# Kernel tuning notes

Hardware: AMD Instinct MI355X
Metric: run time of the kernel (lower is better)

## Reference

```python
import jax, jax.numpy as jnp
import numpy as np

D_MODEL = 2048
N_HEADS = 16
D_HEAD = D_MODEL // N_HEADS
ROPE_BASE = 10000.0
B, L = 2, 2048


def _rope(x, positions):
    # x: [B, H, L, dh]; positions: [B, L] (float)
    dh = x.shape[-1]
    inv_freq = 1.0 / (ROPE_BASE ** (jnp.arange(0, dh, 2, dtype=jnp.float32) / dh))  # [dh/2]
    freqs = positions[:, :, None].astype(jnp.float32) * inv_freq  # [B, L, dh/2]
    cos = jnp.cos(freqs)[:, None, :, :]  # [B, 1, L, dh/2]
    sin = jnp.sin(freqs)[:, None, :, :]
    x1 = x[..., 0::2]
    x2 = x[..., 1::2]
    even = x1 * cos - x2 * sin
    odd = x1 * sin + x2 * cos
    # re-interleave: [..., dh/2, 2] -> [..., dh]
    return jnp.stack([even, odd], axis=-1).reshape(x.shape)


def setup_inputs() -> dict:
    key = jax.random.key(0)
    ks = jax.random.split(key, 5)
    std = 0.02
    x = jax.random.normal(ks[0], (B, L, D_MODEL), dtype=jnp.float32)
    Wq = jax.random.normal(ks[1], (D_MODEL, D_MODEL), dtype=jnp.float32) * std
    Wk = jax.random.normal(ks[2], (D_MODEL, D_MODEL), dtype=jnp.float32) * std
    Wv = jax.random.normal(ks[3], (D_MODEL, D_MODEL), dtype=jnp.float32) * std
    Wo = jax.random.normal(ks[4], (D_MODEL, D_MODEL), dtype=jnp.float32) * (std / np.sqrt(2.0))
    positions = jnp.broadcast_to(jnp.arange(L, dtype=jnp.int32)[None, :], (B, L))
    return {"x": x, "positions": positions, "Wq": Wq, "Wk": Wk, "Wv": Wv, "Wo": Wo}


def reference(x, positions, Wq, Wk, Wv, Wo):
    Bx, Lx, D = x.shape
    H, dh = N_HEADS, D_HEAD
    scale = 1.0 / np.sqrt(dh)
    # torch nn.Linear: y = x @ W.T (weights are [out, in])
    Q = (x @ Wq.T).reshape(Bx, Lx, H, dh).transpose(0, 2, 1, 3)  # [B,H,L,dh]
    K = (x @ Wk.T).reshape(Bx, Lx, H, dh).transpose(0, 2, 1, 3)
    V = (x @ Wv.T).reshape(Bx, Lx, H, dh).transpose(0, 2, 1, 3)
    Q = _rope(Q, positions)
    K = _rope(K, positions)
    scores = jnp.einsum('bhqd,bhkd->bhqk', Q, K) * scale  # [B,H,L,L]
    causal_mask = jnp.triu(jnp.full((Lx, Lx), -jnp.inf, dtype=scores.dtype), k=1)
    scores = scores + causal_mask[None, None, :, :]
    attn = jax.nn.softmax(scores, axis=-1)
    out = jnp.einsum('bhqk,bhkd->bhqd', attn, V)  # [B,H,L,dh]
    out = out.transpose(0, 2, 1, 3).reshape(Bx, Lx, D)
    return out @ Wo.T
```

## Files before the change

kernel.cpp:

```cpp
#include <hip/hip_runtime.h>
#include <hip/hip_bf16.h>

typedef __bf16 bf16;
typedef __bf16 bf16x8 __attribute__((ext_vector_type(8)));
typedef __bf16 bf16x4 __attribute__((ext_vector_type(4)));
typedef float f32x4 __attribute__((ext_vector_type(4)));

#define DM 2048
#define LL 2048
#define NB 2
#define NH 16
#define DH 128

__device__ __forceinline__ void gload_lds16(const void* g, void* l) {
  auto gp = (__attribute__((address_space(1))) void*)(const_cast<void*>(g));
  auto lp = (__attribute__((address_space(3))) void*)l;
  __builtin_amdgcn_global_load_lds(gp, lp, 16, 0, 0);
}

__global__ __launch_bounds__(256) void convert_kernel(
    const float* __restrict__ x, const float* __restrict__ wq,
    const float* __restrict__ wk, const float* __restrict__ wv,
    const float* __restrict__ wo,
    bf16* __restrict__ xb, bf16* __restrict__ wqb, bf16* __restrict__ wkb,
    bf16* __restrict__ wvb, bf16* __restrict__ wob) {
  int i4 = blockIdx.x * 256 + threadIdx.x;
  const float* src;
  bf16* dst;
  int off;
  if (i4 < 2097152) {
    src = x; dst = xb; off = i4;
  } else {
    int t = i4 - 2097152;
    int a = t >> 20;
    off = t & 1048575;
    src = (a == 0) ? wq : (a == 1) ? wk : (a == 2) ? wv : wo;
    dst = (a == 0) ? wqb : (a == 1) ? wkb : (a == 2) ? wvb : wob;
  }
  float4 v = ((const float4*)src)[off];
  bf16x4 o = {(bf16)v.x, (bf16)v.y, (bf16)v.z, (bf16)v.w};
  ((bf16x4*)dst)[off] = o;
}

__global__ __launch_bounds__(256) void rope_table_kernel(float2* __restrict__ cs) {
  int idx = blockIdx.x * 256 + threadIdx.x;
  int pos = idx >> 6, i = idx & 63;
  float inv = powf(10000.0f, -(float)(2 * i) / 128.0f);
  float f = (float)pos * inv;
  cs[idx] = make_float2(cosf(f), sinf(f));
}

template <int MODE>
__global__ __launch_bounds__(256) void gemm_kernel(
    const bf16* __restrict__ A, const bf16* __restrict__ B0,
    const bf16* __restrict__ B1, const bf16* __restrict__ B2,
    bf16* __restrict__ Qh, bf16* __restrict__ Kh, bf16* __restrict__ VT,
    float* __restrict__ Cout, const int* __restrict__ positions,
    const float2* __restrict__ cs) {
  __shared__ __align__(16) bf16 As[128 * 32];
  __shared__ __align__(16) bf16 Bs[128 * 32];
  const int tid = threadIdx.x;
  const int lane = tid & 63;
  const int w = tid >> 6;
  const int wr = w >> 1, wc = w & 1;
  const int lr = lane & 15, lg = lane >> 4;
  const int brow = blockIdx.x * 128;
  const int bcol = blockIdx.y * 128;
  const int z = (MODE == 0) ? (int)blockIdx.z : 0;
  const bf16* Bt = (MODE == 1) ? B0 : (z == 0 ? B0 : (z == 1 ? B1 : B2));

  f32x4 acc[4][4];
#pragma unroll
  for (int m = 0; m < 4; ++m)
#pragma unroll
    for (int n = 0; n < 4; ++n) acc[m][n] = (f32x4){0.f, 0.f, 0.f, 0.f};

  for (int kt = 0; kt < DM / 32; ++kt) {
    __syncthreads();
#pragma unroll
    for (int p = 0; p < 2; ++p) {
      int slot = p * 256 + tid;
      int row = slot >> 2, kq = slot & 3;
      gload_lds16(A + (size_t)(brow + row) * DM + kt * 32 + kq * 8,
                  As + (size_t)(p * 256 + w * 64) * 8);
      gload_lds16(Bt + (size_t)(bcol + row) * DM + kt * 32 + kq * 8,
                  Bs + (size_t)(p * 256 + w * 64) * 8);
    }
    __syncthreads();
    bf16x8 afr[4], bfr[4];
#pragma unroll
    for (int m = 0; m < 4; ++m)
      afr[m] = *(const bf16x8*)(As + (wr * 64 + m * 16 + lr) * 32 + lg * 8);
#pragma unroll
    for (int n = 0; n < 4; ++n)
      bfr[n] = *(const bf16x8*)(Bs + (wc * 64 + n * 16 + lr) * 32 + lg * 8);
#pragma unroll
    for (int m = 0; m < 4; ++m)
#pragma unroll
      for (int n = 0; n < 4; ++n)
        acc[m][n] = __builtin_amdgcn_mfma_f32_16x16x32_bf16(afr[m], bfr[n],
                                                            acc[m][n], 0, 0, 0);
  }

  if (MODE == 1) {
#pragma unroll
    for (int m = 0; m < 4; ++m)
#pragma unroll
      for (int r = 0; r < 4; ++r) {
        int gr = brow + wr * 64 + m * 16 + lg * 4 + r;
#pragma unroll
        for (int n = 0; n < 4; ++n) {
          int j = bcol + wc * 64 + n * 16 + lr;
          Cout[(size_t)gr * DM + j] = acc[m][n][r];
        }
      }
  } else if (z < 2) {
    bf16* Dst = (z == 0) ? Qh : Kh;
#pragma unroll
    for (int m = 0; m < 4; ++m)
#pragma unroll
      for (int r = 0; r < 4; ++r) {
        int gr = brow + wr * 64 + m * 16 + lg * 4 + r;
        int b = gr >> 11, l = gr & (LL - 1);
        int pos = positions[gr];
#pragma unroll
        for (int n = 0; n < 4; ++n) {
          int j = bcol + wc * 64 + n * 16 + lr;
          float v = acc[m][n][r];
          float part = __shfl_xor(v, 1);
          int d = j & 127;
          float2 csv = cs[pos * 64 + (d >> 1)];
          float res = (j & 1) ? (part * csv.y + v * csv.x)
                              : (v * csv.x - part * csv.y);
          Dst[((size_t)(b * NH + (j >> 7)) * LL + l) * DH + d] = (bf16)res;
        }
      }
  } else {
#pragma unroll
    for (int m = 0; m < 4; ++m) {
      int gr0 = brow + wr * 64 + m * 16 + lg * 4;
      int b = gr0 >> 11, l0 = gr0 & (LL - 1);
#pragma unroll
      for (int n = 0; n < 4; ++n) {
        int j = bcol + wc * 64 + n * 16 + lr;
        int d = j & 127, h = j >> 7;
        bf16x4 o = {(bf16)acc[m][n][0], (bf16)acc[m][n][1], (bf16)acc[m][n][2],
                    (bf16)acc[m][n][3]};
        *(bf16x4*)(VT + ((size_t)(b * NH + h) * DH + d) * LL + l0) = o;
      }
    }
  }
}

__global__ __launch_bounds__(256) void attn_kernel(const bf16* __restrict__ Qh,
                                                   const bf16* __restrict__ Kh,
                                                   const bf16* __restrict__ VT,
                                                   bf16* __restrict__ AO) {
  __shared__ __align__(16) bf16 Ks[64 * 128];
  __shared__ __align__(16) bf16 Vs[128 * 64];
  __shared__ __align__(16) bf16 Ps[4][16 * 64];
  const int tid = threadIdx.x;
  const int lane = tid & 63;
  const int w = tid >> 6;
  const int lr = lane & 15, lg = lane >> 4;
  const int bid = blockIdx.x;
  const int xcd = bid & 7;
  const int local = bid >> 3;
  const int bh = xcd * 4 + (local & 3);
  const int q0 = (local >> 2) * 64;
  const int qr0 = q0 + w * 16;
  const bf16* Qb = Qh + (size_t)bh * LL * DH;
  const bf16* Kb = Kh + (size_t)bh * LL * DH;
  const bf16* Vb = VT + (size_t)bh * DH * LL;

  bf16x8 qf[4];
#pragma unroll
  for (int dk = 0; dk < 4; ++dk)
    qf[dk] = *(const bf16x8*)(Qb + (size_t)(qr0 + lr) * DH + dk * 32 + lg * 8);

  float mx[4], ssum[4];
  f32x4 oacc[8];
#pragma unroll
  for (int r = 0; r < 4; ++r) {
    mx[r] = -1e30f;
    ssum[r] = 0.f;
  }
#pragma unroll
  for (int f = 0; f < 8; ++f) oacc[f] = (f32x4){0.f, 0.f, 0.f, 0.f};

  const float scale = 0.08838834764831845f;
  const int kvend = q0 + 64;
  for (int kv0 = 0; kv0 < kvend; kv0 += 64) {
    __syncthreads();
#pragma unroll
    for (int rr = 0; rr < 4; ++rr) {
      int slot = rr * 256 + tid;
      int row = slot >> 4, c = slot & 15;
      gload_lds16(Kb + (size_t)(kv0 + row) * DH + ((c ^ (row & 7)) * 8),
                  Ks + (size_t)(rr * 256 + w * 64) * 8);
    }
#pragma unroll
    for (int rr = 0; rr < 4; ++rr) {
      int slot = rr * 256 + tid;
      int row = slot >> 3, c = slot & 7;
      gload_lds16(Vb + (size_t)row * LL + kv0 + ((c ^ (row & 7)) * 8),
                  Vs + (size_t)(rr * 256 + w * 64) * 8);
    }
    __syncthreads();
    if (kv0 <= qr0 + 15) {
      f32x4 s[4];
#pragma unroll
      for (int n = 0; n < 4; ++n) s[n] = (f32x4){0.f, 0.f, 0.f, 0.f};
#pragma unroll
      for (int n = 0; n < 4; ++n)
#pragma unroll
        for (int dk = 0; dk < 4; ++dk) {
          bf16x8 kf = *(const bf16x8*)(Ks + (n * 16 + lr) * 128 +
                                       (((dk * 4 + lg) ^ (lr & 7)) * 8));
          s[n] = __builtin_amdgcn_mfma_f32_16x16x32_bf16(qf[dk], kf, s[n], 0, 0, 0);
        }
#pragma unroll
      for (int n = 0; n < 4; ++n)
#pragma unroll
        for (int r = 0; r < 4; ++r) {
          int c = kv0 + n * 16 + lr;
          int q = qr0 + lg * 4 + r;
          if (c > q) s[n][r] = -1e30f;
        }
      float pm[4];
      bool ok = true;
#pragma unroll
      for (int r = 0; r < 4; ++r) {
        float tm = fmaxf(fmaxf(s[0][r], s[1][r]), fmaxf(s[2][r], s[3][r]));
        tm = fmaxf(tm, __shfl_xor(tm, 1));
        tm = fmaxf(tm, __shfl_xor(tm, 2));
        tm = fmaxf(tm, __shfl_xor(tm, 4));
        tm = fmaxf(tm, __shfl_xor(tm, 8));
        pm[r] = tm;
        ok = ok && (tm <= mx[r] + 90.0f);
      }
      if (!__all(ok)) {
        float al[4];
#pragma unroll
        for (int r = 0; r < 4; ++r) {
          float mn = fmaxf(mx[r], pm[r]);
          al[r] = __expf((mx[r] - mn) * scale);
          mx[r] = mn;
          ssum[r] *= al[r];
        }
#pragma unroll
        for (int f = 0; f < 8; ++f)
#pragma unroll
          for (int r = 0; r < 4; ++r) oacc[f][r] *= al[r];
      }
#pragma unroll
      for (int r = 0; r < 4; ++r) {
        float t = 0.f;
#pragma unroll
        for (int n = 0; n < 4; ++n) {
          float e = __expf((s[n][r] - mx[r]) * scale);
          s[n][r] = e;
          t += e;
        }
        t += __shfl_xor(t, 1);
        t += __shfl_xor(t, 2);
        t += __shfl_xor(t, 4);
        t += __shfl_xor(t, 8);
        ssum[r] += t;
      }
      bf16* pw = &Ps[w][0];
#pragma unroll
      for (int n = 0; n < 4; ++n)
#pragma unroll
        for (int r = 0; r < 4; ++r) {
          int row = lg * 4 + r;
          int ch = (n * 2 + (lr >> 3)) ^ (row & 7);
          pw[row * 64 + ch * 8 + (lr & 7)] = (bf16)s[n][r];
        }
      asm volatile("s_waitcnt lgkmcnt(0)" ::: "memory");
      __builtin_amdgcn_sched_barrier(0);
#pragma unroll
      for (int kt = 0; kt < 2; ++kt) {
        bf16x8 pf = *(const bf16x8*)(pw + lr * 64 +
                                     (((kt * 4 + lg) ^ (lr & 7)) * 8));
#pragma unroll
        for (int f = 0; f < 8; ++f) {
          bf16x8 vf = *(const bf16x8*)(Vs + (f * 16 + lr) * 64 +
                                       (((kt * 4 + lg) ^ (lr & 7)) * 8));
          oacc[f] = __builtin_amdgcn_mfma_f32_16x16x32_bf16(pf, vf, oacc[f], 0, 0, 0);
        }
      }
    }
  }
  const int b = bh >> 4, h = bh & 15;
#pragma unroll
  for (int f = 0; f < 8; ++f)
#pragma unroll
    for (int r = 0; r < 4; ++r) {
      int q = qr0 + lg * 4 + r;
      float val = oacc[f][r] / ssum[r];
      AO[((size_t)(b * LL + q)) * DM + h * DH + f * 16 + lr] = (bf16)val;
    }
}

extern "C" void kernel_launch(void* const* d_in, const int* in_sizes, int n_in,
                              void* d_out, int out_size, void* d_ws,
                              size_t ws_size, hipStream_t stream) {
  const float* x = (const float*)d_in[0];
  const int* positions = (const int*)d_in[1];
  const float* Wq = (const float*)d_in[2];
  const float* Wk = (const float*)d_in[3];
  const float* Wv = (const float*)d_in[4];
  const float* Wo = (const float*)d_in[5];
  float* out = (float*)d_out;
  char* ws = (char*)d_ws;
  const size_t MB = (size_t)1 << 20;
  bf16* xb = (bf16*)(ws + 0 * MB);
  bf16* wqb = (bf16*)(ws + 16 * MB);
  bf16* wkb = (bf16*)(ws + 24 * MB);
  bf16* wvb = (bf16*)(ws + 32 * MB);
  bf16* wob = (bf16*)(ws + 40 * MB);
  bf16* Qh = (bf16*)(ws + 48 * MB);
  bf16* Kh = (bf16*)(ws + 64 * MB);
  bf16* VTb = (bf16*)(ws + 80 * MB);
  bf16* AO = (bf16*)(ws + 96 * MB);
  float2* cs = (float2*)(ws + 112 * MB);

  convert_kernel<<<dim3(24576), dim3(256), 0, stream>>>(
      x, Wq, Wk, Wv, Wo, xb, wqb, wkb, wvb, wob);
  rope_table_kernel<<<dim3(512), dim3(256), 0, stream>>>(cs);
  gemm_kernel<0><<<dim3(32, 16, 3), dim3(256), 0, stream>>>(
      xb, wqb, wkb, wvb, Qh, Kh, VTb, nullptr, positions, cs);
  attn_kernel<<<dim3(1024), dim3(256), 0, stream>>>(Qh, Kh, VTb, AO);
  gemm_kernel<1><<<dim3(32, 16, 1), dim3(256), 0, stream>>>(
      AO, wob, nullptr, nullptr, nullptr, nullptr, nullptr, out, nullptr,
      nullptr);
}
```

Measured before the change: 450.8 us.

## Double attention query tile per block to reuse K/V tiles across 128 queries

```diff
diff --git a/kernel.cpp b/kernel.cpp
--- a/kernel.cpp
+++ b/kernel.cpp
@@ -158,7 +158,7 @@
                                                    bf16* __restrict__ AO) {
   __shared__ __align__(16) bf16 Ks[64 * 128];
   __shared__ __align__(16) bf16 Vs[128 * 64];
-  __shared__ __align__(16) bf16 Ps[4][16 * 64];
+  __shared__ __align__(16) bf16 Ps[4][32 * 64];
   const int tid = threadIdx.x;
   const int lane = tid & 63;
   const int w = tid >> 6;
@@ -167,29 +167,35 @@
   const int xcd = bid & 7;
   const int local = bid >> 3;
   const int bh = xcd * 4 + (local & 3);
-  const int q0 = (local >> 2) * 64;
-  const int qr0 = q0 + w * 16;
+  const int q0 = (local >> 2) * 128;
+  const int qr0 = q0 + w * 32;
   const bf16* Qb = Qh + (size_t)bh * LL * DH;
   const bf16* Kb = Kh + (size_t)bh * LL * DH;
   const bf16* Vb = VT + (size_t)bh * DH * LL;
 
-  bf16x8 qf[4];
-#pragma unroll
-  for (int dk = 0; dk < 4; ++dk)
-    qf[dk] = *(const bf16x8*)(Qb + (size_t)(qr0 + lr) * DH + dk * 32 + lg * 8);
-
-  float mx[4], ssum[4];
-  f32x4 oacc[8];
-#pragma unroll
-  for (int r = 0; r < 4; ++r) {
-    mx[r] = -1e30f;
-    ssum[r] = 0.f;
-  }
-#pragma unroll
-  for (int f = 0; f < 8; ++f) oacc[f] = (f32x4){0.f, 0.f, 0.f, 0.f};
+  bf16x8 qf[2][4];
+#pragma unroll
+  for (int m = 0; m < 2; ++m)
+#pragma unroll
+    for (int dk = 0; dk < 4; ++dk)
+      qf[m][dk] = *(const bf16x8*)(Qb + (size_t)(qr0 + m * 16 + lr) * DH +
+                                   dk * 32 + lg * 8);
+
+  float mx[2][4], ssum[2][4];
+  f32x4 oacc[2][8];
+#pragma unroll
+  for (int m = 0; m < 2; ++m) {
+#pragma unroll
+    for (int r = 0; r < 4; ++r) {
+      mx[m][r] = -1e30f;
+      ssum[m][r] = 0.f;
+    }
+#pragma unroll
+    for (int f = 0; f < 8; ++f) oacc[m][f] = (f32x4){0.f, 0.f, 0.f, 0.f};
+  }
 
   const float scale = 0.08838834764831845f;
-  const int kvend = q0 + 64;
+  const int kvend = q0 + 128;
   for (int kv0 = 0; kv0 < kvend; kv0 += 64) {
     __syncthreads();
 #pragma unroll
@@ -207,100 +213,120 @@
                   Vs + (size_t)(rr * 256 + w * 64) * 8);
     }
     __syncthreads();
-    if (kv0 <= qr0 + 15) {
-      f32x4 s[4];
-#pragma unroll
-      for (int n = 0; n < 4; ++n) s[n] = (f32x4){0.f, 0.f, 0.f, 0.f};
+    if (kv0 <= qr0 + 31) {
+      f32x4 s[2][4];
+#pragma unroll
+      for (int m = 0; m < 2; ++m)
+#pragma unroll
+        for (int n = 0; n < 4; ++n) s[m][n] = (f32x4){0.f, 0.f, 0.f, 0.f};
 #pragma unroll
       for (int n = 0; n < 4; ++n)
 #pragma unroll
         for (int dk = 0; dk < 4; ++dk) {
           bf16x8 kf = *(const bf16x8*)(Ks + (n * 16 + lr) * 128 +
                                        (((dk * 4 + lg) ^ (lr & 7)) * 8));
-          s[n] = __builtin_amdgcn_mfma_f32_16x16x32_bf16(qf[dk], kf, s[n], 0, 0, 0);
-        }
-#pragma unroll
-      for (int n = 0; n < 4; ++n)
+          s[0][n] = __builtin_amdgcn_mfma_f32_16x16x32_bf16(qf[0][dk], kf,
+                                                            s[0][n], 0, 0, 0);
+          s[1][n] = __builtin_amdgcn_mfma_f32_16x16x32_bf16(qf[1][dk], kf,
+                                                            s[1][n], 0, 0, 0);
+        }
+#pragma unroll
+      for (int m = 0; m < 2; ++m)
+#pragma unroll
+        for (int n = 0; n < 4; ++n)
+#pragma unroll
+          for (int r = 0; r < 4; ++r) {
+            int c = kv0 + n * 16 + lr;
+            int q = qr0 + m * 16 + lg * 4 + r;
+            if (c > q) s[m][n][r] = -1e30f;
+          }
+      float pm[2][4];
+      bool ok = true;
+#pragma unroll
+      for (int m = 0; m < 2; ++m)
 #pragma unroll
         for (int r = 0; r < 4; ++r) {
-          int c = kv0 + n * 16 + lr;
-          int q = qr0 + lg * 4 + r;
-          if (c > q) s[n][r] = -1e30f;
-        }
-      float pm[4];
-      bool ok = true;
-#pragma unroll
-      for (int r = 0; r < 4; ++r) {
-        float tm = fmaxf(fmaxf(s[0][r], s[1][r]), fmaxf(s[2][r], s[3][r]));
-        tm = fmaxf(tm, __shfl_xor(tm, 1));
-        tm = fmaxf(tm, __shfl_xor(tm, 2));
-        tm = fmaxf(tm, __shfl_xor(tm, 4));
-        tm = fmaxf(tm, __shfl_xor(tm, 8));
-        pm[r] = tm;
-        ok = ok && (tm <= mx[r] + 90.0f);
-      }
+          float tm = fmaxf(fmaxf(s[m][0][r], s[m][1][r]),
+                           fmaxf(s[m][2][r], s[m][3][r]));
+          tm = fmaxf(tm, __shfl_xor(tm, 1));
+          tm = fmaxf(tm, __shfl_xor(tm, 2));
+          tm = fmaxf(tm, __shfl_xor(tm, 4));
+          tm = fmaxf(tm, __shfl_xor(tm, 8));
+          pm[m][r] = tm;
+          ok = ok && (tm <= mx[m][r] + 90.0f);
+        }
       if (!__all(ok)) {
-        float al[4];
+#pragma unroll
+        for (int m = 0; m < 2; ++m)
+#pragma unroll
+          for (int r = 0; r < 4; ++r) {
+            float mn = fmaxf(mx[m][r], pm[m][r]);
+            float al = __expf((mx[m][r] - mn) * scale);
+            mx[m][r] = mn;
+            ssum[m][r] *= al;
+#pragma unroll
+            for (int f = 0; f < 8; ++f) oacc[m][f][r] *= al;
+          }
+      }
+#pragma unroll
+      for (int m = 0; m < 2; ++m)
 #pragma unroll
         for (int r = 0; r < 4; ++r) {
-          float mn = fmaxf(mx[r], pm[r]);
-          al[r] = __expf((mx[r] - mn) * scale);
-          mx[r] = mn;
-          ssum[r] *= al[r];
-        }
-#pragma unroll
-        for (int f = 0; f < 8; ++f)
-#pragma unroll
-          for (int r = 0; r < 4; ++r) oacc[f][r] *= al[r];
-      }
-#pragma unroll
-      for (int r = 0; r < 4; ++r) {
-        float t = 0.f;
-#pragma unroll
-        for (int n = 0; n < 4; ++n) {
-          float e = __expf((s[n][r] - mx[r]) * scale);
-          s[n][r] = e;
-          t += e;
-        }
-        t += __shfl_xor(t, 1);
-        t += __shfl_xor(t, 2);
-        t += __shfl_xor(t, 4);
-        t += __shfl_xor(t, 8);
-        ssum[r] += t;
-      }
+          float t = 0.f;
+#pragma unroll
+          for (int n = 0; n < 4; ++n) {
+            float e = __expf((s[m][n][r] - mx[m][r]) * scale);
+            s[m][n][r] = e;
+            t += e;
+          }
+          t += __shfl_xor(t, 1);
+          t += __shfl_xor(t, 2);
+          t += __shfl_xor(t, 4);
+          t += __shfl_xor(t, 8);
+          ssum[m][r] += t;
+        }
       bf16* pw = &Ps[w][0];
 #pragma unroll
-      for (int n = 0; n < 4; ++n)
-#pragma unroll
-        for (int r = 0; r < 4; ++r) {
-          int row = lg * 4 + r;
-          int ch = (n * 2 + (lr >> 3)) ^ (row & 7);
-          pw[row * 64 + ch * 8 + (lr & 7)] = (bf16)s[n][r];
-        }
+      for (int m = 0; m < 2; ++m)
+#pragma unroll
+        for (int n = 0; n < 4; ++n)
+#pragma unroll
+          for (int r = 0; r < 4; ++r) {
+            int row = m * 16 + lg * 4 + r;
+            int ch = (n * 2 + (lr >> 3)) ^ (row & 7);
+            pw[row * 64 + ch * 8 + (lr & 7)] = (bf16)s[m][n][r];
+          }
       asm volatile("s_waitcnt lgkmcnt(0)" ::: "memory");
       __builtin_amdgcn_sched_barrier(0);
 #pragma unroll
       for (int kt = 0; kt < 2; ++kt) {
-        bf16x8 pf = *(const bf16x8*)(pw + lr * 64 +
-                                     (((kt * 4 + lg) ^ (lr & 7)) * 8));
+        bf16x8 pf0 = *(const bf16x8*)(pw + lr * 64 +
+                                      (((kt * 4 + lg) ^ (lr & 7)) * 8));
+        bf16x8 pf1 = *(const bf16x8*)(pw + (16 + lr) * 64 +
+                                      (((kt * 4 + lg) ^ (lr & 7)) * 8));
 #pragma unroll
         for (int f = 0; f < 8; ++f) {
           bf16x8 vf = *(const bf16x8*)(Vs + (f * 16 + lr) * 64 +
                                        (((kt * 4 + lg) ^ (lr & 7)) * 8));
-          oacc[f] = __builtin_amdgcn_mfma_f32_16x16x32_bf16(pf, vf, oacc[f], 0, 0, 0);
+          oacc[0][f] =
+              __builtin_amdgcn_mfma_f32_16x16x32_bf16(pf0, vf, oacc[0][f], 0, 0, 0);
+          oacc[1][f] =
+              __builtin_amdgcn_mfma_f32_16x16x32_bf16(pf1, vf, oacc[1][f], 0, 0, 0);
         }
       }
     }
   }
   const int b = bh >> 4, h = bh & 15;
 #pragma unroll
-  for (int f = 0; f < 8; ++f)
-#pragma unroll
-    for (int r = 0; r < 4; ++r) {
-      int q = qr0 + lg * 4 + r;
-      float val = oacc[f][r] / ssum[r];
-      AO[((size_t)(b * LL + q)) * DM + h * DH + f * 16 + lr] = (bf16)val;
-    }
+  for (int m = 0; m < 2; ++m)
+#pragma unroll
+    for (int f = 0; f < 8; ++f)
+#pragma unroll
+      for (int r = 0; r < 4; ++r) {
+        int q = qr0 + m * 16 + lg * 4 + r;
+        float val = oacc[m][f][r] / ssum[m][r];
+        AO[((size_t)(b * LL + q)) * DM + h * DH + f * 16 + lr] = (bf16)val;
+      }
 }
 
 extern "C" void kernel_launch(void* const* d_in, const int* in_sizes, int n_in,
@@ -331,7 +357,7 @@
   rope_table_kernel<<<dim3(512), dim3(256), 0, stream>>>(cs);
   gemm_kernel<0><<<dim3(32, 16, 3), dim3(256), 0, stream>>>(
       xb, wqb, wkb, wvb, Qh, Kh, VTb, nullptr, positions, cs);
-  attn_kernel<<<dim3(1024), dim3(256), 0, stream>>>(Qh, Kh, VTb, AO);
+  attn_kernel<<<dim3(512), dim3(256), 0, stream>>>(Qh, Kh, VTb, AO);
   gemm_kernel<1><<<dim3(32, 16, 1), dim3(256), 0, stream>>>(
       AO, wob, nullptr, nullptr, nullptr, nullptr, nullptr, out, nullptr,
       nullptr);
```

After: 493.6 us. 1.09x slower.
